# Optimization experiments

Measured on AMD Instinct MI355X. Metric: run time of the kernel, lower is better.

## Reference

```python
import jax, jax.numpy as jnp
import numpy as np
from jax.ops import segment_sum

N_NODES = 300000
N_EDGES = 600000
N_GRAPHS = 12000
HIDDEN = 128
F_ATOM, V_ATOM, D_ATOM = 9, 119, 9
F_BOND, V_BOND, D_BOND = 3, 6, 3


def setup_inputs() -> dict:
    key = jax.random.key(0)
    ks = jax.random.split(key, 12)
    x = jax.random.randint(ks[0], (N_NODES, F_ATOM), 0, 100, dtype=jnp.int64 if jax.config.jax_enable_x64 else jnp.int32)
    edge_index = jax.random.randint(ks[1], (2, N_EDGES), 0, N_NODES)
    edge_attr = jax.random.randint(ks[2], (N_EDGES, F_BOND), 0, 5)
    batch = jnp.sort(jax.random.randint(ks[3], (N_NODES,), 0, N_GRAPHS))
    s = 0.02
    atom_emb = jax.random.normal(ks[4], (F_ATOM, V_ATOM, D_ATOM), jnp.float32) * s
    bond_emb = jax.random.normal(ks[5], (F_BOND, V_BOND, D_BOND), jnp.float32) * s
    W1 = jax.random.normal(ks[6], (D_ATOM, HIDDEN), jnp.float32) * (1.0 / np.sqrt(D_ATOM))
    b1 = jnp.zeros((HIDDEN,), jnp.float32)
    W2 = jax.random.normal(ks[7], (HIDDEN, HIDDEN), jnp.float32) * (1.0 / np.sqrt(HIDDEN))
    b2 = jnp.zeros((HIDDEN,), jnp.float32)
    Wfc = jax.random.normal(ks[8], (HIDDEN, 128), jnp.float32) * (1.0 / np.sqrt(HIDDEN))
    bfc = jnp.zeros((128,), jnp.float32)
    return {"x": x, "edge_index": edge_index, "edge_attr": edge_attr, "batch": batch,
            "atom_emb": atom_emb, "bond_emb": bond_emb,
            "W1": W1, "b1": b1, "W2": W2, "b2": b2, "Wfc": Wfc, "bfc": bfc}


def _multi_embed(tables, idx):
    # tables: [F, V, D], idx: [N, F] -> sum over F of tables[f, idx[:, f]] -> [N, D]
    F = tables.shape[0]
    gathered = tables[jnp.arange(F)[None, :], idx]  # [N, F, D]
    return gathered.sum(axis=1)


def _gcn_conv(h, edge_index, W, b, n_nodes):
    # PyG GCNConv: add self-loops, symmetric deg^-1/2 normalization
    src, dst = edge_index[0], edge_index[1]
    deg = segment_sum(jnp.ones(src.shape[0], h.dtype), dst, num_segments=n_nodes) + 1.0  # self-loop
    dinv = jax.lax.rsqrt(deg)
    h = h @ W  # transform before propagation
    coef = (dinv[src] * dinv[dst])[:, None]
    agg = segment_sum(h[src] * coef, dst, num_segments=n_nodes)
    agg = agg + h * (dinv * dinv)[:, None]  # self-loop contribution (norm = 1/deg)
    return agg + b


def reference(x, edge_index, edge_attr, batch, atom_emb, bond_emb, W1, b1, W2, b2, Wfc, bfc):
    h = _multi_embed(atom_emb, x)            # AtomEncoder: [N, 9]
    _ = _multi_embed(bond_emb, edge_attr)    # BondEncoder (computed, unused downstream)
    h = _gcn_conv(h, edge_index, W1, b1, N_NODES)
    h = jax.nn.relu(h)
    h = _gcn_conv(h, edge_index, W2, b2, N_NODES)
    # global_mean_pool over graphs
    sums = segment_sum(h, batch, num_segments=N_GRAPHS)
    cnt = segment_sum(jnp.ones(N_NODES, h.dtype), batch, num_segments=N_GRAPHS)
    graph_emb = sums / jnp.clip(cnt, 1.0)[:, None]
    return graph_emb @ Wfc + bfc
```

## Files before the change

kernel.cpp:

```cpp
#include <hip/hip_runtime.h>

#define NN 300000
#define NE 600000
#define NG 12000
#define HH 128
#define FA 9
#define VA 119
#define DA 9
#define NCHUNK ((NN + 1023) / 1024)
#define POISON 0xAAAAAAAAu

#define OEMB 0
#define OW1  (FA*VA*DA)
#define OB1  (OW1 + DA*HH)
#define OW2  (OB1 + HH)
#define OB2  (OW2 + HH*HH)
#define OWFC (OB2 + HH)
#define OBFC (OWFC + HH*HH)
#define NWC  (OBFC + HH)

typedef unsigned short u16;
typedef unsigned int u32;
typedef __attribute__((ext_vector_type(8))) short bfrag8;
typedef __attribute__((ext_vector_type(16))) float ffrag16;

__device__ __forceinline__ float bf2f(u16 u){
  union { u32 i; float f; } v; v.i = ((u32)u) << 16; return v.f;
}
__device__ __forceinline__ float bflo(u32 w){
  union { u32 i; float f; } v; v.i = w << 16; return v.f;
}
__device__ __forceinline__ float bfhi(u32 w){
  union { u32 i; float f; } v; v.i = w & 0xFFFF0000u; return v.f;
}
__device__ __forceinline__ u16 f2bf(float f){
  union { float f; u32 i; } v; v.f = f;
  u32 x = v.i;
  return (u16)((x + 0x7FFFu + ((x >> 16) & 1u)) >> 16);
}
__device__ __forceinline__ float ldf(const void* p, int i, int isf32){
  return isf32 ? ((const float*)p)[i] : bf2f(((const u16*)p)[i]);
}
__device__ __forceinline__ int detect_isf32(const u16* emb16, int t, int* scnt){
  if (t == 0) *scnt = 0;
  __syncthreads();
  u16 u = emb16[t];
  int e = (u >> 7) & 0xFF;
  if (e >= 96 && e < 126) atomicAdd(scnt, 1);
  __syncthreads();
  return (*scnt >= 200) ? 0 : 1;
}

__global__ void k_pre(const int* __restrict__ x, const void* emb, const void* W1,
                      const void* b1, const void* W2, const void* b2,
                      const void* Wfc, const void* bfc,
                      const int* __restrict__ batch, const int* __restrict__ dst,
                      int* __restrict__ flag, float* __restrict__ wc,
                      u32* __restrict__ degcur, u16* __restrict__ rank,
                      int* __restrict__ gstart, uint4* __restrict__ h0a,
                      u32* __restrict__ h0b, float* __restrict__ wcomb,
                      float* __restrict__ bcomb, u32* __restrict__ btab2){
  __shared__ float embS[FA * VA * DA];
  __shared__ int scnt;
  int t = threadIdx.x;
  int isf32 = detect_isf32((const u16*)emb, t, &scnt);
  int tid = blockIdx.x * 256 + t;
  int nth = gridDim.x * 256;
  if (tid == 0) flag[0] = isf32;

  {
    int e0 = tid * 2;
    if (e0 < NE){
      u32 r0 = atomicAdd(&degcur[dst[e0]], 1u);
      rank[e0] = (u16)(r0 - POISON);
    }
    if (e0 + 1 < NE){
      u32 r1 = atomicAdd(&degcur[dst[e0 + 1]], 1u);
      rank[e0 + 1] = (u16)(r1 - POISON);
    }
  }

  for (int i = t; i < FA * VA * DA; i += 256) embS[i] = ldf(emb, i, isf32);
  for (int i = tid; i < NWC; i += nth){
    float v;
    if      (i < OW1)  v = ldf(emb, i - OEMB, isf32);
    else if (i < OB1)  v = ldf(W1,  i - OW1,  isf32);
    else if (i < OW2)  v = ldf(b1,  i - OB1,  isf32);
    else if (i < OB2)  v = ldf(W2,  i - OW2,  isf32);
    else if (i < OWFC) v = ldf(b2,  i - OB2,  isf32);
    else if (i < OBFC) v = ldf(Wfc, i - OWFC, isf32);
    else               v = ldf(bfc, i - OBFC, isf32);
    wc[i] = v;
  }

  if (tid < HH * HH){
    int d = tid >> 7, k = tid & 127;
    float s = 0.f;
    #pragma unroll 4
    for (int j = 0; j < HH; ++j) s += ldf(W2, d * HH + j, isf32) * ldf(Wfc, j * HH + k, isf32);
    wcomb[tid] = s;
    if (tid < HH){
      float sb = 0.f;
      #pragma unroll 4
      for (int j = 0; j < HH; ++j) sb += ldf(b2, j, isf32) * ldf(Wfc, j * HH + tid, isf32);
      bcomb[tid] = sb;
    }
    if (tid < 1024){
      int lane = tid >> 4, idx = tid & 15;
      int tile = idx >> 2, reg = idx & 3;
      int half = lane >> 5, col = lane & 31;
      int nn = tile * 32 + col;
      int k0 = half * 8 + reg * 2;
      int k1 = k0 + 1;
      u32 lo = 0, hi = 0;
      if (k0 < 9)       lo = f2bf(ldf(W1, k0 * HH + nn, isf32));
      else if (k0 == 9) lo = f2bf(ldf(b1, nn, isf32));
      if (k1 < 9)       hi = f2bf(ldf(W1, k1 * HH + nn, isf32));
      else if (k1 == 9) hi = f2bf(ldf(b1, nn, isf32));
      btab2[tid] = lo | (hi << 16);
    }
  }

  __syncthreads();
  int n = tid;
  if (n <= NG){
    if (n == NG) gstart[NG] = NN;
    else {
      int lo = 0, hi = NN;
      while (lo < hi){
        int mid = (lo + hi) >> 1;
        if (batch[mid] < n) lo = mid + 1; else hi = mid;
      }
      gstart[n] = lo;
    }
  }
  if (n >= NN) return;
  int idx[FA];
  #pragma unroll
  for (int f = 0; f < FA; ++f) idx[f] = x[n * FA + f];
  float acc[DA];
  #pragma unroll
  for (int d = 0; d < DA; ++d){
    float a = 0.f;
    #pragma unroll
    for (int f = 0; f < FA; ++f) a += embS[(f * VA + idx[f]) * DA + d];
    acc[d] = a;
  }
  uint4 pv;
  pv.x = (u32)f2bf(acc[0]) | ((u32)f2bf(acc[1]) << 16);
  pv.y = (u32)f2bf(acc[2]) | ((u32)f2bf(acc[3]) << 16);
  pv.z = (u32)f2bf(acc[4]) | ((u32)f2bf(acc[5]) << 16);
  pv.w = (u32)f2bf(acc[6]) | ((u32)f2bf(acc[7]) << 16);
  h0a[n] = pv;
  h0b[n] = (u32)f2bf(acc[8]);
}

__global__ void k_scan1(const u32* __restrict__ degp, int* __restrict__ rowoff,
                        float* __restrict__ dinv, int* __restrict__ part){
  __shared__ int sh[256];
  int base = blockIdx.x * 1024;
  int t = threadIdx.x;
  int i0 = base + t * 4;
  int v0=0, v1=0, v2=0, v3=0;
  if (i0 + 0 < NN){ v0 = (int)(degp[i0 + 0] - POISON); dinv[i0 + 0] = rsqrtf((float)v0 + 1.0f); }
  if (i0 + 1 < NN){ v1 = (int)(degp[i0 + 1] - POISON); dinv[i0 + 1] = rsqrtf((float)v1 + 1.0f); }
  if (i0 + 2 < NN){ v2 = (int)(degp[i0 + 2] - POISON); dinv[i0 + 2] = rsqrtf((float)v2 + 1.0f); }
  if (i0 + 3 < NN){ v3 = (int)(degp[i0 + 3] - POISON); dinv[i0 + 3] = rsqrtf((float)v3 + 1.0f); }
  int tsum = v0 + v1 + v2 + v3;
  sh[t] = tsum;
  __syncthreads();
  for (int off = 1; off < 256; off <<= 1){
    int add = (t >= off) ? sh[t - off] : 0;
    __syncthreads();
    sh[t] += add;
    __syncthreads();
  }
  int run = sh[t] - tsum;
  if (t == 255) part[blockIdx.x] = sh[255];
  if (i0 + 0 <= NN) rowoff[i0 + 0] = run;
  run += v0;
  if (i0 + 1 <= NN) rowoff[i0 + 1] = run;
  run += v1;
  if (i0 + 2 <= NN) rowoff[i0 + 2] = run;
  run += v2;
  if (i0 + 3 <= NN) rowoff[i0 + 3] = run;
}

__global__ void k_scan2(int* __restrict__ part){
  __shared__ int sh[512];
  int t = threadIdx.x;
  int v = (t < NCHUNK) ? part[t] : 0;
  sh[t] = v;
  __syncthreads();
  for (int off = 1; off < 512; off <<= 1){
    int add = (t >= off) ? sh[t - off] : 0;
    __syncthreads();
    sh[t] += add;
    __syncthreads();
  }
  if (t < NCHUNK) part[t] = sh[t] - v;
}

#define GROW(i) (rowoff[(i)] + part[(u32)(i) >> 10])

__global__ void k_fill(const int* __restrict__ src, const int* __restrict__ dst,
                       const u16* __restrict__ rank, const int* __restrict__ rowoff,
                       const int* __restrict__ part, const float* __restrict__ dinv,
                       uint2* __restrict__ csr){
  int e = blockIdx.x * 256 + threadIdx.x;
  if (e < NE){
    int s = src[e], d = dst[e];
    int pos = GROW(d) + (int)rank[e];
    uint2 ent;
    ent.x = (u32)s;
    ent.y = __float_as_uint(dinv[s] * dinv[d]);
    csr[pos] = ent;
  }
}

__global__ void k_l1csr(const uint4* __restrict__ h0a, const u32* __restrict__ h0b,
                        uint4* __restrict__ agg1a, u32* __restrict__ agg1b,
                        const int* __restrict__ rowoff, const int* __restrict__ part,
                        const uint2* __restrict__ csr, const float* __restrict__ dinv){
  int n = blockIdx.x * 256 + threadIdx.x;
  if (n >= NN) return;
  float di = dinv[n];
  float c0 = di * di;
  float acc[DA];
  {
    uint4 ra = h0a[n];
    u32 r4 = h0b[n];
    acc[0]=c0*bflo(ra.x); acc[1]=c0*bfhi(ra.x); acc[2]=c0*bflo(ra.y); acc[3]=c0*bfhi(ra.y);
    acc[4]=c0*bflo(ra.z); acc[5]=c0*bfhi(ra.z); acc[6]=c0*bflo(ra.w); acc[7]=c0*bfhi(ra.w);
    acc[8]=c0*bflo(r4);
  }
  int s0 = GROW(n), s1 = GROW(n + 1);
  #pragma unroll 2
  for (int j = s0; j < s1; ++j){
    uint2 ent = csr[j];
    int s = (int)ent.x;
    float c = __uint_as_float(ent.y);
    uint4 ra = h0a[s];
    u32 r4 = h0b[s];
    acc[0]+=c*bflo(ra.x); acc[1]+=c*bfhi(ra.x); acc[2]+=c*bflo(ra.y); acc[3]+=c*bfhi(ra.y);
    acc[4]+=c*bflo(ra.z); acc[5]+=c*bfhi(ra.z); acc[6]+=c*bflo(ra.w); acc[7]+=c*bfhi(ra.w);
    acc[8]+=c*bflo(r4);
  }
  uint4 pv;
  pv.x = (u32)f2bf(acc[0]) | ((u32)f2bf(acc[1]) << 16);
  pv.y = (u32)f2bf(acc[2]) | ((u32)f2bf(acc[3]) << 16);
  pv.z = (u32)f2bf(acc[4]) | ((u32)f2bf(acc[5]) << 16);
  pv.w = (u32)f2bf(acc[6]) | ((u32)f2bf(acc[7]) << 16);
  agg1a[n] = pv;
  agg1b[n] = (u32)f2bf(acc[8]) | (0x3F80u << 16);
}

__global__ void k_l2pool(const uint4* __restrict__ agg1a, const u32* __restrict__ agg1b,
                         const float* __restrict__ dinv,
                         const int* __restrict__ rowoff, const int* __restrict__ part,
                         const uint2* __restrict__ csr, const int* __restrict__ gstart,
                         const u32* __restrict__ btab2, float* __restrict__ pooled){
  int t = threadIdx.x;
  int g = blockIdx.x * 4 + (t >> 6);
  int lane = t & 63;
  if (g >= NG) return;
  u32 bf[16];
  {
    const u32* bp = btab2 + lane * 16;
    #pragma unroll
    for (int i = 0; i < 16; ++i) bf[i] = bp[i];
  }
  int a = gstart[g], b = gstart[g + 1];
  int j0 = GROW(a), j1 = GROW(b);
  int nself = b - a;
  int M = nself + (j1 - j0);
  float s[4] = {0.f, 0.f, 0.f, 0.f};
  int half = lane >> 5;
  int li = lane & 31;

  for (int base = 0; base < M; base += 32){
    int i = base + li;
    u32 a0 = 0, a1 = 0, a2 = 0, a3 = 0;
    float coef = 0.f;
    if (i < M){
      int n;
      if (i < nself){
        n = a + i;
        float dn = dinv[n];
        coef = dn * dn;
      } else {
        uint2 e = csr[j0 + (i - nself)];
        n = (int)e.x;
        coef = __uint_as_float(e.y);
      }
      if (half == 0){
        uint4 ra = agg1a[n];
        a0 = ra.x; a1 = ra.y; a2 = ra.z; a3 = ra.w;
      } else {
        a0 = agg1b[n];
      }
    }
    float cf[16];
    #pragma unroll
    for (int reg = 0; reg < 16; ++reg){
      int row = (reg & 3) + 8 * (reg >> 2) + 4 * half;
      cf[reg] = __shfl(coef, row, 64);
    }
    union { u32 u[4]; bfrag8 v; } au;
    au.u[0] = a0; au.u[1] = a1; au.u[2] = a2; au.u[3] = a3;
    #pragma unroll
    for (int tile = 0; tile < 4; ++tile){
      union { u32 u[4]; bfrag8 v; } bu;
      bu.u[0] = bf[tile*4+0]; bu.u[1] = bf[tile*4+1];
      bu.u[2] = bf[tile*4+2]; bu.u[3] = bf[tile*4+3];
      ffrag16 c;
      #pragma unroll
      for (int q = 0; q < 16; ++q) c[q] = 0.f;
      c = __builtin_amdgcn_mfma_f32_32x32x16_bf16(au.v, bu.v, c, 0, 0, 0);
      float acc = 0.f;
      #pragma unroll
      for (int reg = 0; reg < 16; ++reg)
        acc += fmaxf(c[reg], 0.f) * cf[reg];
      s[tile] += acc;
    }
  }
  #pragma unroll
  for (int tile = 0; tile < 4; ++tile){
    float v = s[tile];
    v += __shfl_xor(v, 32, 64);
    s[tile] = v;
  }
  if (half == 0){
    #pragma unroll
    for (int tile = 0; tile < 4; ++tile)
      pooled[(size_t)g * HH + tile * 32 + li] = s[tile];
  }
}

__global__ void k_head(const float* __restrict__ pooled, const float* __restrict__ wcomb,
                       const float* __restrict__ bcomb, const float* __restrict__ wc,
                       const int* __restrict__ gstart, const int* __restrict__ flag,
                       void* __restrict__ out){
  __shared__ float wS[HH * HH];
  __shared__ float pl[2][HH];
  int t = threadIdx.x;
  for (int i = t; i < HH * HH; i += 256) wS[i] = wcomb[i];
  __syncthreads();
  int isf32 = flag[0];
  int gg = t >> 7, k = t & 127;
  for (int p = blockIdx.x; p < NG / 2; p += gridDim.x){
    int g = p * 2 + gg;
    int cnt = gstart[g + 1] - gstart[g];
    float inv = 1.0f / (float)(cnt > 1 ? cnt : 1);
    pl[gg][k] = pooled[(size_t)g * HH + k] * inv;
    __syncthreads();
    float acc = wc[OBFC + k] + (cnt > 0 ? bcomb[k] : 0.f);
    #pragma unroll 8
    for (int d = 0; d < HH; ++d) acc += pl[gg][d] * wS[d * HH + k];
    if (isf32) ((float*)out)[(size_t)g * HH + k] = acc;
    else       ((u16*)out)[(size_t)g * HH + k] = f2bf(acc);
    __syncthreads();
  }
}

extern "C" void kernel_launch(void* const* d_in, const int* in_sizes, int n_in,
                              void* d_out, int out_size, void* d_ws, size_t ws_size,
                              hipStream_t stream){
  const int* x     = (const int*)d_in[0];
  const int* ei    = (const int*)d_in[1];
  const int* batch = (const int*)d_in[3];
  const void* aemb = d_in[4];
  const void* W1   = d_in[6];
  const void* b1   = d_in[7];
  const void* W2   = d_in[8];
  const void* b2   = d_in[9];
  const void* Wfc  = d_in[10];
  const void* bfc  = d_in[11];
  const int* srcp = ei;
  const int* dstp = ei + NE;

  char* p = (char*)d_ws;
  int*   flag   = (int*)p;                 p += 64;
  float* wc     = (float*)p;               p += sizeof(float) * 43944;
  float* wcomb  = (float*)p;               p += sizeof(float) * (HH * HH);
  float* bcomb  = (float*)p;               p += sizeof(float) * HH;
  u32*   btab2  = (u32*)p;                 p += sizeof(u32) * 1024;
  u32*   degcur = (u32*)p;                 p += sizeof(u32) * (NN + 16);
  int*   rowoff = (int*)p;                 p += sizeof(int) * (NN + 4);
  int*   part   = (int*)p;                 p += sizeof(int) * 512;
  float* dinv   = (float*)p;               p += sizeof(float) * NN;
  u16*   rank   = (u16*)p;                 p += sizeof(u16) * (NE + 8);
  uint2* csr    = (uint2*)p;               p += sizeof(uint2) * NE;
  int*   gstart = (int*)p;                 p += sizeof(int) * (NG + 4);
  float* pooled = (float*)p;               p += sizeof(float) * (size_t)NG * HH;
  uint4* h0a    = (uint4*)p;               p += sizeof(uint4) * NN;
  u32*   h0b    = (u32*)p;                 p += sizeof(u32) * NN;
  uint4* agg1a  = (uint4*)p;               p += sizeof(uint4) * NN;
  u32*   agg1b  = (u32*)p;                 p += sizeof(u32) * NN;
  (void)p; (void)ws_size; (void)n_in; (void)in_sizes; (void)out_size;

  k_pre   <<<(NN + 255) / 256, 256, 0, stream>>>(x, aemb, W1, b1, W2, b2, Wfc, bfc,
                                                 batch, dstp, flag, wc, degcur, rank,
                                                 gstart, h0a, h0b, wcomb, bcomb, btab2);
  k_scan1 <<<NCHUNK, 256, 0, stream>>>(degcur, rowoff, dinv, part);
  k_scan2 <<<1, 512, 0, stream>>>(part);
  k_fill  <<<(NE + 255) / 256, 256, 0, stream>>>(srcp, dstp, rank, rowoff, part, dinv, csr);
  k_l1csr <<<(NN + 255) / 256, 256, 0, stream>>>(h0a, h0b, agg1a, agg1b, rowoff, part, csr, dinv);
  k_l2pool<<<NG / 4, 256, 0, stream>>>(agg1a, agg1b, dinv, rowoff, part, csr, gstart,
                                       btab2, pooled);
  k_head  <<<1500, 256, 0, stream>>>(pooled, wcomb, bcomb, wc, gstart, flag, d_out);
}
```

Baseline: 241.6 us.

## Replace global atomic degree counting with per-block LDS histogram kernel

```diff
diff --git a/kernel.cpp b/kernel.cpp
--- a/kernel.cpp
+++ b/kernel.cpp
@@ -10,6 +10,9 @@
 #define NCHUNK ((NN + 1023) / 1024)
 #define POISON 0xAAAAAAAAu
 
+#define CH 2048
+#define NBH ((NN + CH - 1) / CH)
+
 #define OEMB 0
 #define OW1  (FA*VA*DA)
 #define OB1  (OW1 + DA*HH)
@@ -51,12 +54,36 @@
   return (*scnt >= 200) ? 0 : 1;
 }
 
+__global__ void __launch_bounds__(1024)
+k_hist(const int* __restrict__ dst, u32* __restrict__ deg, u16* __restrict__ rank){
+  __shared__ u32 cnt[CH];
+  int t = threadIdx.x;
+  u32 base = (u32)(blockIdx.x * CH);
+  for (int i = t; i < CH; i += 1024) cnt[i] = 0;
+  __syncthreads();
+  const int4* d4 = (const int4*)dst;
+  #pragma unroll 2
+  for (int i = t; i < NE / 4; i += 1024){
+    int4 v = d4[i];
+    int e = i * 4;
+    u32 r;
+    r = (u32)v.x - base; if (r < CH) rank[e    ] = (u16)atomicAdd(&cnt[r], 1u);
+    r = (u32)v.y - base; if (r < CH) rank[e + 1] = (u16)atomicAdd(&cnt[r], 1u);
+    r = (u32)v.z - base; if (r < CH) rank[e + 2] = (u16)atomicAdd(&cnt[r], 1u);
+    r = (u32)v.w - base; if (r < CH) rank[e + 3] = (u16)atomicAdd(&cnt[r], 1u);
+  }
+  __syncthreads();
+  for (int i = t; i < CH; i += 1024){
+    int n = (int)base + i;
+    if (n < NN) deg[n] = cnt[i];
+  }
+}
+
 __global__ void k_pre(const int* __restrict__ x, const void* emb, const void* W1,
                       const void* b1, const void* W2, const void* b2,
                       const void* Wfc, const void* bfc,
-                      const int* __restrict__ batch, const int* __restrict__ dst,
+                      const int* __restrict__ batch,
                       int* __restrict__ flag, float* __restrict__ wc,
-                      u32* __restrict__ degcur, u16* __restrict__ rank,
                       int* __restrict__ gstart, uint4* __restrict__ h0a,
                       u32* __restrict__ h0b, float* __restrict__ wcomb,
                       float* __restrict__ bcomb, u32* __restrict__ btab2){
@@ -67,18 +94,6 @@
   int tid = blockIdx.x * 256 + t;
   int nth = gridDim.x * 256;
   if (tid == 0) flag[0] = isf32;
-
-  {
-    int e0 = tid * 2;
-    if (e0 < NE){
-      u32 r0 = atomicAdd(&degcur[dst[e0]], 1u);
-      rank[e0] = (u16)(r0 - POISON);
-    }
-    if (e0 + 1 < NE){
-      u32 r1 = atomicAdd(&degcur[dst[e0 + 1]], 1u);
-      rank[e0 + 1] = (u16)(r1 - POISON);
-    }
-  }
 
   for (int i = t; i < FA * VA * DA; i += 256) embS[i] = ldf(emb, i, isf32);
   for (int i = tid; i < NWC; i += nth){
@@ -162,10 +177,10 @@
   int t = threadIdx.x;
   int i0 = base + t * 4;
   int v0=0, v1=0, v2=0, v3=0;
-  if (i0 + 0 < NN){ v0 = (int)(degp[i0 + 0] - POISON); dinv[i0 + 0] = rsqrtf((float)v0 + 1.0f); }
-  if (i0 + 1 < NN){ v1 = (int)(degp[i0 + 1] - POISON); dinv[i0 + 1] = rsqrtf((float)v1 + 1.0f); }
-  if (i0 + 2 < NN){ v2 = (int)(degp[i0 + 2] - POISON); dinv[i0 + 2] = rsqrtf((float)v2 + 1.0f); }
-  if (i0 + 3 < NN){ v3 = (int)(degp[i0 + 3] - POISON); dinv[i0 + 3] = rsqrtf((float)v3 + 1.0f); }
+  if (i0 + 0 < NN){ v0 = (int)degp[i0 + 0]; dinv[i0 + 0] = rsqrtf((float)v0 + 1.0f); }
+  if (i0 + 1 < NN){ v1 = (int)degp[i0 + 1]; dinv[i0 + 1] = rsqrtf((float)v1 + 1.0f); }
+  if (i0 + 2 < NN){ v2 = (int)degp[i0 + 2]; dinv[i0 + 2] = rsqrtf((float)v2 + 1.0f); }
+  if (i0 + 3 < NN){ v3 = (int)degp[i0 + 3]; dinv[i0 + 3] = rsqrtf((float)v3 + 1.0f); }
   int tsum = v0 + v1 + v2 + v3;
   sh[t] = tsum;
   __syncthreads();
@@ -399,9 +414,10 @@
   u32*   agg1b  = (u32*)p;                 p += sizeof(u32) * NN;
   (void)p; (void)ws_size; (void)n_in; (void)in_sizes; (void)out_size;
 
+  k_hist  <<<NBH, 1024, 0, stream>>>(dstp, degcur, rank);
   k_pre   <<<(NN + 255) / 256, 256, 0, stream>>>(x, aemb, W1, b1, W2, b2, Wfc, bfc,
-                                                 batch, dstp, flag, wc, degcur, rank,
-                                                 gstart, h0a, h0b, wcomb, bcomb, btab2);
+                                                 batch, flag, wc, gstart, h0a, h0b,
+                                                 wcomb, bcomb, btab2);
   k_scan1 <<<NCHUNK, 256, 0, stream>>>(degcur, rowoff, dinv, part);
   k_scan2 <<<1, 512, 0, stream>>>(part);
   k_fill  <<<(NE + 255) / 256, 256, 0, stream>>>(srcp, dstp, rank, rowoff, part, dinv, csr);
```

After: 285.1 us. 1.18x slower.

## Split degree-count atomics into dedicated blocks with vectorized dst loads

Applied to the files above, without the earlier changes.

```diff
diff --git a/kernel.cpp b/kernel.cpp
--- a/kernel.cpp
+++ b/kernel.cpp
@@ -9,6 +9,9 @@
 #define DA 9
 #define NCHUNK ((NN + 1023) / 1024)
 #define POISON 0xAAAAAAAAu
+
+#define HB  64
+#define NCB 1172
 
 #define OEMB 0
 #define OW1  (FA*VA*DA)
@@ -63,22 +66,29 @@
   __shared__ float embS[FA * VA * DA];
   __shared__ int scnt;
   int t = threadIdx.x;
+
+  if (blockIdx.x < HB){
+    int htid = blockIdx.x * 256 + t;
+    const int4* d4 = (const int4*)dst;
+    uint2* r2 = (uint2*)rank;
+    for (int i = htid; i < NE / 4; i += HB * 256){
+      int4 v = d4[i];
+      u32 r0 = atomicAdd(&degcur[v.x], 1u);
+      u32 r1 = atomicAdd(&degcur[v.y], 1u);
+      u32 rr2 = atomicAdd(&degcur[v.z], 1u);
+      u32 rr3 = atomicAdd(&degcur[v.w], 1u);
+      uint2 pk;
+      pk.x = (u32)(u16)(r0 - POISON) | (((u32)(u16)(r1 - POISON)) << 16);
+      pk.y = (u32)(u16)(rr2 - POISON) | (((u32)(u16)(rr3 - POISON)) << 16);
+      r2[i] = pk;
+    }
+    return;
+  }
+
   int isf32 = detect_isf32((const u16*)emb, t, &scnt);
-  int tid = blockIdx.x * 256 + t;
-  int nth = gridDim.x * 256;
+  int tid = (blockIdx.x - HB) * 256 + t;
+  int nth = NCB * 256;
   if (tid == 0) flag[0] = isf32;
-
-  {
-    int e0 = tid * 2;
-    if (e0 < NE){
-      u32 r0 = atomicAdd(&degcur[dst[e0]], 1u);
-      rank[e0] = (u16)(r0 - POISON);
-    }
-    if (e0 + 1 < NE){
-      u32 r1 = atomicAdd(&degcur[dst[e0 + 1]], 1u);
-      rank[e0 + 1] = (u16)(r1 - POISON);
-    }
-  }
 
   for (int i = t; i < FA * VA * DA; i += 256) embS[i] = ldf(emb, i, isf32);
   for (int i = tid; i < NWC; i += nth){
@@ -399,14 +409,14 @@
   u32*   agg1b  = (u32*)p;                 p += sizeof(u32) * NN;
   (void)p; (void)ws_size; (void)n_in; (void)in_sizes; (void)out_size;
 
-  k_pre   <<<(NN + 255) / 256, 256, 0, stream>>>(x, aemb, W1, b1, W2, b2, Wfc, bfc,
-                                                 batch, dstp, flag, wc, degcur, rank,
-                                                 gstart, h0a, h0b, wcomb, bcomb, btab2);
+  k_pre   <<<HB + NCB, 256, 0, stream>>>(x, aemb, W1, b1, W2, b2, Wfc, bfc,
+                                         batch, dstp, flag, wc, degcur, rank,
+                                         gstart, h0a, h0b, wcomb, bcomb, btab2);
   k_scan1 <<<NCHUNK, 256, 0, stream>>>(degcur, rowoff, dinv, part);
   k_scan2 <<<1, 512, 0, stream>>>(part);
   k_fill  <<<(NE + 255) / 256, 256, 0, stream>>>(srcp, dstp, rank, rowoff, part, dinv, csr);
   k_l1csr <<<(NN + 255) / 256, 256, 0, stream>>>(h0a, h0b, agg1a, agg1b, rowoff, part, csr, dinv);
   k_l2pool<<<NG / 4, 256, 0, stream>>>(agg1a, agg1b, dinv, rowoff, part, csr, gstart,
                                        btab2, pooled);
-  k_head  <<<1500, 256, 0, stream>>>(pooled, wcomb, bcomb, wc, gstart, flag, d_out);
-}
+  k_head  <<<512, 256, 0, stream>>>(pooled, wcomb, bcomb, wc, gstart, flag, d_out);
+}
```

Measured after the change: 219.2 us. 9.3% less time.
